# Kernel optimization log

Measured on AMD Instinct MI355X. Metric: run time of the kernel, lower is better.

Reference implementation:

```python
import jax, jax.numpy as jnp
import numpy as np

HEADS = 4
HEAD_DIM = 32
DIM = 256
HIDDEN = HEADS * HEAD_DIM  # 128
SCALE = HEAD_DIM ** -0.5


def rmsnorm(x, g):
    # channel-wise L2 normalize (dim=1) * g * sqrt(C), lucidrains-style RMSNorm for conv maps
    inv = jax.lax.rsqrt(jnp.sum(x * x, axis=1, keepdims=True) + 1e-12)
    return x * inv * (g * (x.shape[1] ** 0.5))[None, :, None, None]


def setup_inputs() -> dict:
    key = jax.random.key(0)
    k1, k2, k3 = jax.random.split(key, 3)
    b, H, W = 16, 64, 64
    x = jax.random.normal(k1, (b, DIM, H, W), dtype=jnp.float32)
    W_qkv = jax.random.normal(k2, (3 * HIDDEN, DIM), dtype=jnp.float32) * (DIM ** -0.5)
    W_out = jax.random.normal(k3, (DIM, HIDDEN), dtype=jnp.float32) * (HIDDEN ** -0.5)
    b_out = jnp.zeros((DIM,), dtype=jnp.float32)
    g_norm = jnp.ones((DIM,), dtype=jnp.float32)
    g_out = jnp.ones((DIM,), dtype=jnp.float32)
    return {"x": x, "W_qkv": W_qkv, "W_out": W_out, "b_out": b_out,
            "g_norm": g_norm, "g_out": g_out}


def reference(x, W_qkv, W_out, b_out, g_norm, g_out):
    b, c, H, W = x.shape
    n = H * W
    xn = rmsnorm(x, g_norm)
    # 1x1 conv projection to q,k,v: (b, 3*hidden, H, W)
    qkv = jnp.einsum('bchw,oc->bohw', xn, W_qkv)
    qkv = qkv.reshape(b, 3, HEADS, HEAD_DIM, n)
    q, k, v = qkv[:, 0], qkv[:, 1], qkv[:, 2]  # (b, h, d, n)
    q = jax.nn.softmax(q, axis=-2)  # over head_dim
    k = jax.nn.softmax(k, axis=-1)  # over tokens
    # context: (b, h, d, e)
    context = jnp.einsum('bhdn,bhen->bhde', k, v)
    out = jnp.einsum('bhde,bhdn->bhen', context, q) * SCALE  # (b, h, e, n)
    out = out.reshape(b, HIDDEN, H, W)
    out = jnp.einsum('bchw,oc->bohw', out, W_out) + b_out[None, :, None, None]
    return rmsnorm(out, g_out)
```

## Files before the change

kernel.cpp:

```cpp
#include <hip/hip_runtime.h>


typedef _Float16 half8 __attribute__((ext_vector_type(8)));
typedef _Float16 half4 __attribute__((ext_vector_type(4)));
typedef float f32x4 __attribute__((ext_vector_type(4)));

#define SCALE_F 0.17677669529663687f

#define GLOAD16(g, s) __builtin_amdgcn_global_load_lds( \
    (const __attribute__((address_space(1))) void*)(g), \
    (__attribute__((address_space(3))) void*)(s), 16, 0, 0)

__global__ __launch_bounds__(256) void k1_prep(const float* __restrict__ x,
                                               const float* __restrict__ g_norm,
                                               const float* __restrict__ W_qkv,
                                               const float* __restrict__ W_out,
                                               _Float16* __restrict__ W16,
                                               _Float16* __restrict__ Wo16,
                                               _Float16* __restrict__ x_t) {
  const int t = threadIdx.x;
  if (blockIdx.x == 64) {
    #pragma unroll
    for (int i = 0; i < 8; ++i) {
      int idx = blockIdx.y * 2048 + i * 256 + t;
      f32x4 v;
      if (idx < 24576) v = *(const f32x4*)(W_qkv + (size_t)idx * 4);
      else             v = *(const f32x4*)(W_out + (size_t)(idx - 24576) * 4);
      half4 h = {(_Float16)v[0], (_Float16)v[1], (_Float16)v[2], (_Float16)v[3]};
      if (idx < 24576) *(half4*)(W16 + (size_t)idx * 4) = h;
      else             *(half4*)(Wo16 + (size_t)(idx - 24576) * 4) = h;
    }
    return;
  }
  const int b = blockIdx.y;
  const int p0 = blockIdx.x * 64;
  __shared__ _Float16 tile[256][68];
  __shared__ float g16s[256];
  __shared__ float psum[64][4];
  __shared__ float sinv[64];
  g16s[t] = g_norm[t] * 16.0f;
  const float* xb = x + (size_t)b * 256 * 4096;
  #pragma unroll
  for (int it = 0; it < 16; ++it) {
    int c = it * 16 + (t >> 4);
    int px = (t & 15) * 4;
    f32x4 v = *(const f32x4*)(xb + (size_t)c * 4096 + p0 + px);
    half4 h = {(_Float16)v[0], (_Float16)v[1], (_Float16)v[2], (_Float16)v[3]};
    *(half4*)&tile[c][px] = h;
  }
  __syncthreads();
  {
    int px = t & 63, q = t >> 6;
    float s = 0.f;
    #pragma unroll
    for (int i = 0; i < 64; ++i) {
      float f = (float)tile[q * 64 + i][px];
      s += f * f;
    }
    psum[px][q] = s;
  }
  __syncthreads();
  if (t < 64) {
    float s = psum[t][0] + psum[t][1] + psum[t][2] + psum[t][3];
    sinv[t] = rsqrtf(s + 1e-12f);
  }
  __syncthreads();
  _Float16* xt = x_t + ((size_t)b * 4096 + p0) * 256;
  #pragma unroll
  for (int j = 0; j < 8; ++j) {
    int idx8 = t + 256 * j;
    int px = idx8 >> 5;
    int c8 = (idx8 & 31) * 8;
    float iv = sinv[px];
    half8 h;
    #pragma unroll
    for (int i = 0; i < 8; ++i)
      h[i] = (_Float16)((float)tile[c8 + i][px] * iv * g16s[c8 + i]);
    *(half8*)(xt + (size_t)px * 256 + c8) = h;
  }
}

__global__ __launch_bounds__(256, 3) void k2_fused(const _Float16* __restrict__ W16,
                                                   const _Float16* __restrict__ x_t,
                                                   _Float16* __restrict__ qhat,
                                                   float* __restrict__ ctxp,
                                                   float* __restrict__ sumep) {
  const int pt = blockIdx.x, b = blockIdx.y;
  const int p0 = pt * 64;
  const int t = threadIdx.x;
  const int h = t >> 6, l = t & 63;
  const int lg = l >> 4, ll = l & 15;
  __shared__ __align__(1024) char smem[49152];
  char* xbuf = smem;
  char* r2 = smem + 32768;
  char* vt = smem;

  const _Float16* Xbase = x_t + ((size_t)b * 4096 + p0) * 256;
  #pragma unroll
  for (int i = 0; i < 8; ++i) {
    int q = i * 256 + t;
    int px = q >> 5, c = q & 31;
    GLOAD16(Xbase + (size_t)px * 256 + (c ^ (px & 15)) * 8, smem + q * 16);
  }
  half8 af[8][2];
  #pragma unroll
  for (int ks = 0; ks < 8; ++ks)
    #pragma unroll
    for (int mf = 0; mf < 2; ++mf)
      af[ks][mf] = *(const half8*)(W16 + (size_t)(h * 32 + mf * 16 + ll) * 256 + ks * 32 + lg * 8);
  __syncthreads();

  const f32x4 fz = {0.f, 0.f, 0.f, 0.f};
  #pragma unroll
  for (int mt = 0; mt < 3; ++mt) {
    f32x4 acc[2][4];
    #pragma unroll
    for (int i = 0; i < 2; ++i)
      #pragma unroll
      for (int j = 0; j < 4; ++j) acc[i][j] = fz;
    #pragma unroll
    for (int ks = 0; ks < 8; ++ks) {
      half8 bf[4];
      #pragma unroll
      for (int nf = 0; nf < 4; ++nf) {
        int px = nf * 16 + ll;
        bf[nf] = *(const half8*)(xbuf + px * 512 + (((ks * 4 + lg) ^ ll) << 4));
      }
      #pragma unroll
      for (int mf = 0; mf < 2; ++mf)
        #pragma unroll
        for (int nf = 0; nf < 4; ++nf)
          acc[mf][nf] = __builtin_amdgcn_mfma_f32_16x16x32_f16(af[ks][mf], bf[nf], acc[mf][nf], 0, 0, 0);
    }
    if (mt < 2) {
      const _Float16* Wn = W16 + (size_t)((mt + 1) * 128 + h * 32) * 256;
      #pragma unroll
      for (int ks = 0; ks < 8; ++ks)
        #pragma unroll
        for (int mf = 0; mf < 2; ++mf)
          af[ks][mf] = *(const half8*)(Wn + (size_t)(mf * 16 + ll) * 256 + ks * 32 + lg * 8);
    }
    if (mt == 0) {
      float s[4] = {0.f, 0.f, 0.f, 0.f};
      #pragma unroll
      for (int mf = 0; mf < 2; ++mf)
        #pragma unroll
        for (int nf = 0; nf < 4; ++nf)
          #pragma unroll
          for (int rr = 0; rr < 4; ++rr) {
            float v = __expf(acc[mf][nf][rr]);
            acc[mf][nf][rr] = v;
            s[nf] += v;
          }
      #pragma unroll
      for (int nf = 0; nf < 4; ++nf) {
        s[nf] += __shfl_xor(s[nf], 16);
        s[nf] += __shfl_xor(s[nf], 32);
        s[nf] = 1.0f / s[nf];
      }
      #pragma unroll
      for (int mf = 0; mf < 2; ++mf)
        #pragma unroll
        for (int nf = 0; nf < 4; ++nf) {
          int px = nf * 16 + ll;
          int cphys = (h * 4 + mf * 2 + (lg >> 1)) ^ (px & 15);
          half4 hv;
          #pragma unroll
          for (int rr = 0; rr < 4; ++rr) hv[rr] = (_Float16)(acc[mf][nf][rr] * s[nf]);
          *(half4*)(r2 + px * 256 + (cphys << 4) + (lg & 1) * 8) = hv;
        }
      __syncthreads();
      _Float16* qb = qhat + ((size_t)b * 4096 + p0) * 128;
      #pragma unroll
      for (int i = 0; i < 4; ++i) {
        int q = i * 256 + t;
        int px = q >> 4, g = q & 15;
        half8 hv = *(const half8*)(r2 + px * 256 + ((g ^ (px & 15)) << 4));
        *(half8*)(qb + (size_t)px * 128 + g * 8) = hv;
      }
      __syncthreads();
    } else if (mt == 1) {
      float rs[2][4];
      #pragma unroll
      for (int mf = 0; mf < 2; ++mf)
        #pragma unroll
        for (int rr = 0; rr < 4; ++rr) rs[mf][rr] = 0.f;
      #pragma unroll
      for (int mf = 0; mf < 2; ++mf)
        #pragma unroll
        for (int nf = 0; nf < 4; ++nf)
          #pragma unroll
          for (int rr = 0; rr < 4; ++rr) {
            float v = __expf(acc[mf][nf][rr] - 10.f);
            acc[mf][nf][rr] = v;
            rs[mf][rr] += v;
          }
      #pragma unroll
      for (int mf = 0; mf < 2; ++mf)
        #pragma unroll
        for (int rr = 0; rr < 4; ++rr) {
          float v = rs[mf][rr];
          v += __shfl_xor(v, 1);
          v += __shfl_xor(v, 2);
          v += __shfl_xor(v, 4);
          v += __shfl_xor(v, 8);
          rs[mf][rr] = v;
        }
      if (ll == 0) {
        #pragma unroll
        for (int mf = 0; mf < 2; ++mf)
          #pragma unroll
          for (int rr = 0; rr < 4; ++rr)
            sumep[((size_t)b * 128 + h * 32 + mf * 16 + lg * 4 + rr) * 64 + pt] = rs[mf][rr];
      }
      #pragma unroll
      for (int mf = 0; mf < 2; ++mf)
        #pragma unroll
        for (int nf = 0; nf < 4; ++nf)
          #pragma unroll
          for (int rr = 0; rr < 4; ++rr) {
            int ch = h * 32 + mf * 16 + lg * 4 + rr;
            int px = nf * 16 + ll;
            *(_Float16*)(r2 + ch * 128 + (((px >> 3) ^ (ch & 7)) << 4) + (px & 7) * 2) =
                (_Float16)acc[mf][nf][rr];
          }
    } else {
      __syncthreads();
      #pragma unroll
      for (int mf = 0; mf < 2; ++mf)
        #pragma unroll
        for (int nf = 0; nf < 4; ++nf)
          #pragma unroll
          for (int rr = 0; rr < 4; ++rr) {
            int ch = h * 32 + mf * 16 + lg * 4 + rr;
            int px = nf * 16 + ll;
            *(_Float16*)(vt + ch * 128 + (((px >> 3) ^ (ch & 7)) << 4) + (px & 7) * 2) =
                (_Float16)acc[mf][nf][rr];
          }
      f32x4 ca[2][2] = {{fz, fz}, {fz, fz}};
      #pragma unroll
      for (int ks2 = 0; ks2 < 2; ++ks2) {
        half8 a2[2], b2[2];
        #pragma unroll
        for (int ti = 0; ti < 2; ++ti) {
          int ra = h * 32 + ti * 16 + ll;
          int cc = (ks2 * 4 + lg) ^ (ra & 7);
          a2[ti] = *(const half8*)(r2 + ra * 128 + (cc << 4));
          b2[ti] = *(const half8*)(vt + ra * 128 + (cc << 4));
        }
        #pragma unroll
        for (int ti = 0; ti < 2; ++ti)
          #pragma unroll
          for (int tj = 0; tj < 2; ++tj)
            ca[ti][tj] = __builtin_amdgcn_mfma_f32_16x16x32_f16(a2[ti], b2[tj], ca[ti][tj], 0, 0, 0);
      }
      float* cp = ctxp + (size_t)(((b * 64 + pt) * 4) + h) * 1024;
      #pragma unroll
      for (int ti = 0; ti < 2; ++ti)
        #pragma unroll
        for (int tj = 0; tj < 2; ++tj)
          #pragma unroll
          for (int rr = 0; rr < 4; ++rr)
            cp[(ti * 16 + lg * 4 + rr) * 32 + tj * 16 + ll] = ca[ti][tj][rr];
    }
  }
}

__global__ __launch_bounds__(256) void k3_reduce(const float* __restrict__ ctxp,
                                                 const float* __restrict__ sumep,
                                                 float* __restrict__ ctx,
                                                 float* __restrict__ sume) {
  const int sl = blockIdx.x, b = blockIdx.y;
  const int t = threadIdx.x;
  if (sl == 0 && t < 128) {
    float s = 0.f;
    const float* sp = sumep + ((size_t)b * 128 + t) * 64;
    #pragma unroll 8
    for (int pt = 0; pt < 64; ++pt) s += sp[pt];
    sume[b * 128 + t] = s;
  }
  float a = 0.f;
  const float* p = ctxp + (size_t)b * 64 * 4096 + sl * 256 + t;
  #pragma unroll 8
  for (int pt = 0; pt < 64; ++pt) a += p[(size_t)pt * 4096];
  ctx[(size_t)b * 4096 + sl * 256 + t] = a;
}

__global__ __launch_bounds__(256) void k4b_fold(const _Float16* __restrict__ Wo16,
                                                const float* __restrict__ ctx,
                                                const float* __restrict__ sumexp,
                                                _Float16* __restrict__ M) {
  const int mq = blockIdx.x, b = blockIdx.y;
  const int t = threadIdx.x;
  const int h = t >> 6, l = t & 63;
  const int m0 = mq * 64;
  const float* cb = ctx + (size_t)(b * 4 + h) * 1024;
  const float* sb = sumexp + b * 128 + h * 32;
  half8 bf[2];
  #pragma unroll
  for (int n0 = 0; n0 < 2; ++n0) {
    int d = n0 * 16 + (l & 15);
    float s = SCALE_F / sb[d];
    const float* ce = cb + d * 32 + (l >> 4) * 8;
    half8 hb;
    #pragma unroll
    for (int j = 0; j < 8; ++j) hb[j] = (_Float16)(ce[j] * s);
    bf[n0] = hb;
  }
  const f32x4 fz = {0.f, 0.f, 0.f, 0.f};
  _Float16* Mb = M + (size_t)(b * 256) * 128;
  #pragma unroll
  for (int mf = 0; mf < 4; ++mf) {
    int row = m0 + mf * 16 + (l & 15);
    half8 af = *(const half8*)(Wo16 + (size_t)row * 128 + h * 32 + (l >> 4) * 8);
    #pragma unroll
    for (int n0 = 0; n0 < 2; ++n0) {
      f32x4 c = __builtin_amdgcn_mfma_f32_16x16x32_f16(af, bf[n0], fz, 0, 0, 0);
      #pragma unroll
      for (int rr = 0; rr < 4; ++rr) {
        int r = m0 + mf * 16 + (l >> 4) * 4 + rr;
        Mb[(size_t)r * 128 + h * 32 + n0 * 16 + (l & 15)] = (_Float16)c[rr];
      }
    }
  }
}

__global__ __launch_bounds__(256) void k5c_out(const _Float16* __restrict__ M,
                                               const _Float16* __restrict__ qhat,
                                               const float* __restrict__ b_out,
                                               const float* __restrict__ g_out,
                                               float* __restrict__ out) {
  const int pt = blockIdx.x, b = blockIdx.y;
  const int p0 = pt * 64;
  const int t = threadIdx.x;
  const int wid = t >> 6, l = t & 63;
  __shared__ __align__(16) char smem[81920];
  float* rp = (float*)smem;
  float* bo = (float*)(smem + 69632);
  float* g16o = (float*)(smem + 70656);
  float* psum = (float*)(smem + 71680);
  float* sinvp = (float*)(smem + 72704);
  const _Float16* Mb = M + (size_t)b * 256 * 128;
  const _Float16* Qb = qhat + ((size_t)b * 4096 + p0) * 128;
  #pragma unroll
  for (int i = 0; i < 16; ++i) {
    int ci = t + 256 * i;
    int r = ci >> 4, c = ci & 15;
    *(half8*)(smem + r * 256 + ((c ^ (r & 15)) << 4)) = *(const half8*)(Mb + (size_t)r * 128 + c * 8);
  }
  #pragma unroll
  for (int i = 0; i < 4; ++i) {
    int ci = t + 256 * i;
    int r = ci >> 4, c = ci & 15;
    *(half8*)(smem + 65536 + r * 256 + ((c ^ (r & 15)) << 4)) = *(const half8*)(Qb + (size_t)r * 128 + c * 8);
  }
  __syncthreads();
  const f32x4 fz = {0.f, 0.f, 0.f, 0.f};
  f32x4 acc[4][4];
  #pragma unroll
  for (int i = 0; i < 4; ++i)
    #pragma unroll
    for (int j = 0; j < 4; ++j) acc[i][j] = fz;
  #pragma unroll
  for (int kk = 0; kk < 4; ++kk) {
    half8 af[4], bf[4];
    int ck = kk * 4 + (l >> 4);
    #pragma unroll
    for (int mf = 0; mf < 4; ++mf) {
      int r = wid * 64 + mf * 16 + (l & 15);
      af[mf] = *(const half8*)(smem + r * 256 + ((ck ^ (r & 15)) << 4));
    }
    #pragma unroll
    for (int nf = 0; nf < 4; ++nf) {
      int r = nf * 16 + (l & 15);
      bf[nf] = *(const half8*)(smem + 65536 + r * 256 + ((ck ^ (r & 15)) << 4));
    }
    #pragma unroll
    for (int mf = 0; mf < 4; ++mf)
      #pragma unroll
      for (int nf = 0; nf < 4; ++nf)
        acc[mf][nf] = __builtin_amdgcn_mfma_f32_16x16x32_f16(af[mf], bf[nf], acc[mf][nf], 0, 0, 0);
  }
  __syncthreads();
  bo[t] = b_out[t];
  g16o[t] = g_out[t] * 16.0f;
  #pragma unroll
  for (int mf = 0; mf < 4; ++mf)
    #pragma unroll
    for (int nf = 0; nf < 4; ++nf)
      #pragma unroll
      for (int rr = 0; rr < 4; ++rr) {
        int r = wid * 64 + mf * 16 + (l >> 4) * 4 + rr;
        int px = nf * 16 + (l & 15);
        rp[r * 68 + px] = acc[mf][nf][rr];
      }
  __syncthreads();
  {
    int px = t & 63, q = t >> 6;
    float s = 0.f;
    #pragma unroll
    for (int i = 0; i < 64; ++i) {
      int r = q * 64 + i;
      float f = rp[r * 68 + px] + bo[r];
      s += f * f;
    }
    psum[px * 4 + q] = s;
  }
  __syncthreads();
  if (t < 64)
    sinvp[t] = rsqrtf(psum[t * 4] + psum[t * 4 + 1] + psum[t * 4 + 2] + psum[t * 4 + 3] + 1e-12f);
  __syncthreads();
  float* ob = out + (size_t)(b * 256) * 4096 + p0;
  #pragma unroll
  for (int i = 0; i < 16; ++i) {
    int idx4 = t + 256 * i;
    int r = idx4 >> 4, px4 = (idx4 & 15) * 4;
    f32x4 v;
    #pragma unroll
    for (int ii = 0; ii < 4; ++ii)
      v[ii] = (rp[r * 68 + px4 + ii] + bo[r]) * sinvp[px4 + ii] * g16o[r];
    *(f32x4*)(ob + (size_t)r * 4096 + px4) = v;
  }
}

extern "C" void kernel_launch(void* const* d_in, const int* in_sizes, int n_in,
                              void* d_out, int out_size, void* d_ws, size_t ws_size,
                              hipStream_t stream) {
  const float* x      = (const float*)d_in[0];
  const float* W_qkv  = (const float*)d_in[1];
  const float* W_out  = (const float*)d_in[2];
  const float* b_out  = (const float*)d_in[3];
  const float* g_norm = (const float*)d_in[4];
  const float* g_out  = (const float*)d_in[5];
  float* out = (float*)d_out;
  char* ws = (char*)d_ws;
  if (ws_size < 69214208) return;

  _Float16* W16   = (_Float16*)(ws);
  _Float16* x_t   = (_Float16*)(ws + 196608);
  _Float16* qhat  = (_Float16*)(ws + 33751040);
  float*    ctx   = (float*)(ws + 50528256);
  float*    sume  = (float*)(ws + 50790400);
  _Float16* M     = (_Float16*)(ws + 50798592);
  _Float16* Wo16  = (_Float16*)(ws + 51847168);
  float*    ctxp  = (float*)(ws + 51912704);
  float*    sumep = (float*)(ws + 68689920);

  k1_prep<<<dim3(65, 16), 256, 0, stream>>>(x, g_norm, W_qkv, W_out, W16, Wo16, x_t);
  k2_fused<<<dim3(64, 16), 256, 0, stream>>>(W16, x_t, qhat, ctxp, sumep);
  k3_reduce<<<dim3(16, 16), 256, 0, stream>>>(ctxp, sumep, ctx, sume);
  k4b_fold<<<dim3(4, 16), 256, 0, stream>>>(Wo16, ctx, sume, M);
  k5c_out<<<dim3(64, 16), 256, 0, stream>>>(M, qhat, b_out, g_out, out);
}
```

Before: 92.07 us.

## Fuse input RMSNorm and fp16 transpose into QKV projection kernel

The prep kernel no longer normalizes x and writes a transposed fp16 copy. The projection kernel now reads fp32 x directly, converts it, and transposes it into swizzled LDS. It computes per-pixel inverse norms there and applies them after the MFMA as a per-column scale, with g_norm folded into the fp16 QKV weights. This removes a full write and re-read of a 32 MB intermediate, at the cost of scattered 2-byte LDS stores, extra barriers, and a small fp16 precision difference from scaling after the matmul.

```diff
diff --git a/kernel.cpp b/kernel.cpp
--- a/kernel.cpp
+++ b/kernel.cpp
@@ -11,96 +11,61 @@
     (const __attribute__((address_space(1))) void*)(g), \
     (__attribute__((address_space(3))) void*)(s), 16, 0, 0)
 
-__global__ __launch_bounds__(256) void k1_prep(const float* __restrict__ x,
-                                               const float* __restrict__ g_norm,
-                                               const float* __restrict__ W_qkv,
-                                               const float* __restrict__ W_out,
-                                               _Float16* __restrict__ W16,
-                                               _Float16* __restrict__ Wo16,
-                                               _Float16* __restrict__ x_t) {
+__global__ __launch_bounds__(256) void kW(const float* __restrict__ W_qkv,
+                                          const float* __restrict__ W_out,
+                                          const float* __restrict__ g_norm,
+                                          _Float16* __restrict__ W16,
+                                          _Float16* __restrict__ Wo16) {
   const int t = threadIdx.x;
-  if (blockIdx.x == 64) {
-    #pragma unroll
-    for (int i = 0; i < 8; ++i) {
-      int idx = blockIdx.y * 2048 + i * 256 + t;
-      f32x4 v;
-      if (idx < 24576) v = *(const f32x4*)(W_qkv + (size_t)idx * 4);
-      else             v = *(const f32x4*)(W_out + (size_t)(idx - 24576) * 4);
+  __shared__ float g16s[256];
+  g16s[t] = g_norm[t] * 16.0f;
+  __syncthreads();
+  #pragma unroll
+  for (int i = 0; i < 8; ++i) {
+    int idx = blockIdx.x * 2048 + i * 256 + t;
+    if (idx < 24576) {
+      f32x4 v = *(const f32x4*)(W_qkv + (size_t)idx * 4);
+      int c0 = (idx & 63) * 4;
+      half4 h = {(_Float16)(v[0] * g16s[c0]), (_Float16)(v[1] * g16s[c0 + 1]),
+                 (_Float16)(v[2] * g16s[c0 + 2]), (_Float16)(v[3] * g16s[c0 + 3])};
+      *(half4*)(W16 + (size_t)idx * 4) = h;
+    } else {
+      f32x4 v = *(const f32x4*)(W_out + (size_t)(idx - 24576) * 4);
       half4 h = {(_Float16)v[0], (_Float16)v[1], (_Float16)v[2], (_Float16)v[3]};
-      if (idx < 24576) *(half4*)(W16 + (size_t)idx * 4) = h;
-      else             *(half4*)(Wo16 + (size_t)(idx - 24576) * 4) = h;
-    }
-    return;
-  }
-  const int b = blockIdx.y;
-  const int p0 = blockIdx.x * 64;
-  __shared__ _Float16 tile[256][68];
-  __shared__ float g16s[256];
-  __shared__ float psum[64][4];
-  __shared__ float sinv[64];
-  g16s[t] = g_norm[t] * 16.0f;
-  const float* xb = x + (size_t)b * 256 * 4096;
-  #pragma unroll
-  for (int it = 0; it < 16; ++it) {
-    int c = it * 16 + (t >> 4);
-    int px = (t & 15) * 4;
-    f32x4 v = *(const f32x4*)(xb + (size_t)c * 4096 + p0 + px);
-    half4 h = {(_Float16)v[0], (_Float16)v[1], (_Float16)v[2], (_Float16)v[3]};
-    *(half4*)&tile[c][px] = h;
-  }
-  __syncthreads();
-  {
-    int px = t & 63, q = t >> 6;
-    float s = 0.f;
-    #pragma unroll
-    for (int i = 0; i < 64; ++i) {
-      float f = (float)tile[q * 64 + i][px];
-      s += f * f;
-    }
-    psum[px][q] = s;
-  }
-  __syncthreads();
-  if (t < 64) {
-    float s = psum[t][0] + psum[t][1] + psum[t][2] + psum[t][3];
-    sinv[t] = rsqrtf(s + 1e-12f);
-  }
-  __syncthreads();
-  _Float16* xt = x_t + ((size_t)b * 4096 + p0) * 256;
-  #pragma unroll
-  for (int j = 0; j < 8; ++j) {
-    int idx8 = t + 256 * j;
-    int px = idx8 >> 5;
-    int c8 = (idx8 & 31) * 8;
-    float iv = sinv[px];
-    half8 h;
-    #pragma unroll
-    for (int i = 0; i < 8; ++i)
-      h[i] = (_Float16)((float)tile[c8 + i][px] * iv * g16s[c8 + i]);
-    *(half8*)(xt + (size_t)px * 256 + c8) = h;
-  }
-}
-
-__global__ __launch_bounds__(256, 3) void k2_fused(const _Float16* __restrict__ W16,
-                                                   const _Float16* __restrict__ x_t,
-                                                   _Float16* __restrict__ qhat,
-                                                   float* __restrict__ ctxp,
-                                                   float* __restrict__ sumep) {
+      *(half4*)(Wo16 + (size_t)(idx - 24576) * 4) = h;
+    }
+  }
+}
+
+__global__ __launch_bounds__(256, 3) void k2_mega(const _Float16* __restrict__ W16,
+                                                  const float* __restrict__ x,
+                                                  _Float16* __restrict__ qhat,
+                                                  float* __restrict__ ctxp,
+                                                  float* __restrict__ sumep) {
   const int pt = blockIdx.x, b = blockIdx.y;
   const int p0 = pt * 64;
   const int t = threadIdx.x;
   const int h = t >> 6, l = t & 63;
   const int lg = l >> 4, ll = l & 15;
-  __shared__ __align__(1024) char smem[49152];
+  __shared__ __align__(1024) char smem[50432];
   char* xbuf = smem;
   char* r2 = smem + 32768;
   char* vt = smem;
-
-  const _Float16* Xbase = x_t + ((size_t)b * 4096 + p0) * 256;
-  #pragma unroll
-  for (int i = 0; i < 8; ++i) {
-    int q = i * 256 + t;
-    int px = q >> 5, c = q & 31;
-    GLOAD16(Xbase + (size_t)px * 256 + (c ^ (px & 15)) * 8, smem + q * 16);
+  float* psum = (float*)(smem + 49152);
+  float* sinvp = (float*)(smem + 50176);
+
+  const float* xb = x + ((size_t)b * 256) * 4096 + p0;
+  #pragma unroll
+  for (int it = 0; it < 16; ++it) {
+    int ch = it * 16 + (t >> 4);
+    int px4 = (t & 15) * 4;
+    f32x4 v = *(const f32x4*)(xb + (size_t)ch * 4096 + px4);
+    int c = ch >> 3, o = ch & 7;
+    #pragma unroll
+    for (int j = 0; j < 4; ++j) {
+      int px = px4 + j;
+      *(_Float16*)(xbuf + px * 512 + ((c ^ (px & 15)) << 4) + o * 2) = (_Float16)v[j];
+    }
   }
   half8 af[8][2];
   #pragma unroll
@@ -109,6 +74,24 @@
     for (int mf = 0; mf < 2; ++mf)
       af[ks][mf] = *(const half8*)(W16 + (size_t)(h * 32 + mf * 16 + ll) * 256 + ks * 32 + lg * 8);
   __syncthreads();
+  {
+    float s = 0.f;
+    #pragma unroll
+    for (int i = 0; i < 8; ++i) {
+      int c = h * 8 + i;
+      half8 hv = *(const half8*)(xbuf + l * 512 + ((c ^ (l & 15)) << 4));
+      #pragma unroll
+      for (int j = 0; j < 8; ++j) { float f = (float)hv[j]; s += f * f; }
+    }
+    psum[l * 4 + h] = s;
+  }
+  __syncthreads();
+  if (t < 64)
+    sinvp[t] = rsqrtf(psum[t * 4] + psum[t * 4 + 1] + psum[t * 4 + 2] + psum[t * 4 + 3] + 1e-12f);
+  __syncthreads();
+  float sv[4];
+  #pragma unroll
+  for (int nf = 0; nf < 4; ++nf) sv[nf] = sinvp[nf * 16 + ll];
 
   const f32x4 fz = {0.f, 0.f, 0.f, 0.f};
   #pragma unroll
@@ -122,10 +105,8 @@
     for (int ks = 0; ks < 8; ++ks) {
       half8 bf[4];
       #pragma unroll
-      for (int nf = 0; nf < 4; ++nf) {
-        int px = nf * 16 + ll;
-        bf[nf] = *(const half8*)(xbuf + px * 512 + (((ks * 4 + lg) ^ ll) << 4));
-      }
+      for (int nf = 0; nf < 4; ++nf)
+        bf[nf] = *(const half8*)(xbuf + (nf * 16 + ll) * 512 + (((ks * 4 + lg) ^ ll) << 4));
       #pragma unroll
       for (int mf = 0; mf < 2; ++mf)
         #pragma unroll
@@ -148,7 +129,7 @@
         for (int nf = 0; nf < 4; ++nf)
           #pragma unroll
           for (int rr = 0; rr < 4; ++rr) {
-            float v = __expf(acc[mf][nf][rr]);
+            float v = __expf(acc[mf][nf][rr] * sv[nf]);
             acc[mf][nf][rr] = v;
             s[nf] += v;
           }
@@ -191,7 +172,7 @@
         for (int nf = 0; nf < 4; ++nf)
           #pragma unroll
           for (int rr = 0; rr < 4; ++rr) {
-            float v = __expf(acc[mf][nf][rr] - 10.f);
+            float v = __expf(acc[mf][nf][rr] * sv[nf] - 10.f);
             acc[mf][nf][rr] = v;
             rs[mf][rr] += v;
           }
@@ -235,7 +216,7 @@
             int ch = h * 32 + mf * 16 + lg * 4 + rr;
             int px = nf * 16 + ll;
             *(_Float16*)(vt + ch * 128 + (((px >> 3) ^ (ch & 7)) << 4) + (px & 7) * 2) =
-                (_Float16)acc[mf][nf][rr];
+                (_Float16)(acc[mf][nf][rr] * sv[nf]);
           }
       f32x4 ca[2][2] = {{fz, fz}, {fz, fz}};
       #pragma unroll
@@ -434,20 +415,19 @@
   const float* g_out  = (const float*)d_in[5];
   float* out = (float*)d_out;
   char* ws = (char*)d_ws;
-  if (ws_size < 69214208) return;
+  if (ws_size < 35659776) return;
 
   _Float16* W16   = (_Float16*)(ws);
-  _Float16* x_t   = (_Float16*)(ws + 196608);
-  _Float16* qhat  = (_Float16*)(ws + 33751040);
-  float*    ctx   = (float*)(ws + 50528256);
-  float*    sume  = (float*)(ws + 50790400);
-  _Float16* M     = (_Float16*)(ws + 50798592);
-  _Float16* Wo16  = (_Float16*)(ws + 51847168);
-  float*    ctxp  = (float*)(ws + 51912704);
-  float*    sumep = (float*)(ws + 68689920);
-
-  k1_prep<<<dim3(65, 16), 256, 0, stream>>>(x, g_norm, W_qkv, W_out, W16, Wo16, x_t);
-  k2_fused<<<dim3(64, 16), 256, 0, stream>>>(W16, x_t, qhat, ctxp, sumep);
+  _Float16* Wo16  = (_Float16*)(ws + 196608);
+  _Float16* qhat  = (_Float16*)(ws + 262144);
+  float*    ctx   = (float*)(ws + 17039360);
+  float*    sume  = (float*)(ws + 17301504);
+  _Float16* M     = (_Float16*)(ws + 17309696);
+  float*    ctxp  = (float*)(ws + 18358272);
+  float*    sumep = (float*)(ws + 35135488);
+
+  kW<<<16, 256, 0, stream>>>(W_qkv, W_out, g_norm, W16, Wo16);
+  k2_mega<<<dim3(64, 16), 256, 0, stream>>>(W16, x, qhat, ctxp, sumep);
   k3_reduce<<<dim3(16, 16), 256, 0, stream>>>(ctxp, sumep, ctx, sume);
   k4b_fold<<<dim3(4, 16), 256, 0, stream>>>(Wo16, ctx, sume, M);
   k5c_out<<<dim3(64, 16), 256, 0, stream>>>(M, qhat, b_out, g_out, out);
```

Measured after the change: 80.19 us. -12.9%, faster.
